# Optimization experiments

Hardware: AMD Instinct MI355X
Metric: run time of the kernel (lower is better)

## Reference

```python
import jax, jax.numpy as jnp
import numpy as np

B, T, D, H, K, V, W = 2, 2048, 1024, 16, 64, 64, 256
BANK = 64
CUE = 50250
EPS = 1e-6
SCALE = K ** -0.5
LOCAL_SCALE = 0.3
ROPE_BASE = 10000.0


def setup_inputs() -> dict:
    key = jax.random.key(0)
    ks = jax.random.split(key, 13)
    s = 0.02
    return {
        "x": jax.random.normal(ks[0], (B, T, D), jnp.float32),
        "gdn_state": jax.random.normal(ks[1], (B, H, K, V), jnp.float32),
        "input_ids": jax.random.randint(ks[2], (B, T), 0, 50320),
        "key_bank": jax.random.normal(ks[3], (H, BANK, K), jnp.float32),
        "norm_w": jnp.ones((D,), jnp.float32),
        "wq": jax.random.normal(ks[4], (D, D), jnp.float32) * s,
        "wk": jax.random.normal(ks[5], (D, D), jnp.float32) * s,
        "wv": jax.random.normal(ks[6], (D, D), jnp.float32) * s,
        "wo": jax.random.normal(ks[7], (D, D), jnp.float32) * s,
        "w_gq": jax.random.normal(ks[8], (H * K, D), jnp.float32) * s,
        "w_ro": jax.random.normal(ks[9], (D, H * V), jnp.float32) * s,
        "w_gate": jax.random.normal(ks[10], (H, D), jnp.float32) * s,
        "b_gate": jnp.ones((H,), jnp.float32),
    }


def _rope(u):
    # u: [B, T, H, K]
    inv_freq = 1.0 / (ROPE_BASE ** (jnp.arange(0, K, 2, dtype=jnp.float32) / K))
    t = jnp.arange(T, dtype=jnp.float32)
    freqs = t[:, None] * inv_freq[None, :]            # [T, K/2]
    emb = jnp.concatenate([freqs, freqs], axis=-1)    # [T, K]
    cos = jnp.cos(emb)[None, :, None, :]
    sin = jnp.sin(emb)[None, :, None, :]
    u1, u2 = u[..., : K // 2], u[..., K // 2 :]
    rotated = jnp.concatenate([-u2, u1], axis=-1)
    return u * cos + rotated * sin


def reference(x, gdn_state, input_ids, key_bank, norm_w, wq, wk, wv, wo,
              w_gq, w_ro, w_gate, b_gate):
    # RMSNorm
    rms = jnp.sqrt(jnp.mean(x * x, axis=-1, keepdims=True) + EPS)
    x_norm = x / rms * norm_w

    # QKV projections -> [B, T, H, K]
    q = (x_norm @ wq.T).reshape(B, T, H, K)
    k = (x_norm @ wk.T).reshape(B, T, H, K)
    v = (x_norm @ wv.T).reshape(B, T, H, K)
    q = _rope(q)
    k = _rope(k)

    # Causal sliding-window attention (PyTorch fallback math: full TxT + band mask)
    scores = jnp.einsum("bthk,bshk->bhts", q, k) * SCALE  # [B, H, T, T]
    i = jnp.arange(T)
    allowed = (i[None, :] <= i[:, None]) & (i[None, :] >= i[:, None] - W)  # [T, T]
    scores = jnp.where(allowed[None, None], scores, jnp.float32(-jnp.inf))
    probs = jax.nn.softmax(scores, axis=-1)
    local = jnp.einsum("bhts,bshv->bthv", probs, v).reshape(B, T, D)
    local = LOCAL_SCALE * (local @ wo.T)  # eval path: local_scale * o_proj(local_out)

    # Global retrieval from GDN state
    q_g = (x_norm @ w_gq.T).reshape(B, T, H, K)
    # CUE token override: positions with input_ids == CUE + idx use key_bank[:, idx, :]
    idx = input_ids - CUE                              # [B, T]
    valid = (idx >= 0) & (idx < BANK)
    ci = jnp.clip(idx, 0, BANK - 1)
    gathered = key_bank.transpose(1, 0, 2)[ci]         # [B, T, H, K]
    q_g = jnp.where(valid[..., None, None], gathered, q_g)

    retrieved = jnp.einsum("bhkv,bthk->bthv", gdn_state, q_g).reshape(B, T, H * V)
    retrieval_out = retrieved @ w_ro.T                 # [B, T, D]
    gate = jax.nn.sigmoid(x_norm @ w_gate.T + b_gate)  # [B, T, H]
    retrieval_out = jnp.mean(gate, axis=-1, keepdims=True) * retrieval_out

    return x + local + retrieval_out
```

## Files before the change

### kernel.cpp

```cpp
#include <hip/hip_runtime.h>
#include <cstddef>

typedef __bf16 bf16_t;
typedef __bf16 bf16x8 __attribute__((ext_vector_type(8)));
typedef __bf16 bf16x4 __attribute__((ext_vector_type(4)));
typedef float  f32x4  __attribute__((ext_vector_type(4)));

__global__ __launch_bounds__(256) void rmsnorm_gate(const float* __restrict__ x,
                                                    const float* __restrict__ w,
                                                    const float* __restrict__ wg,
                                                    const float* __restrict__ bg,
                                                    bf16_t* __restrict__ xn,
                                                    float* __restrict__ gm) {
  int t = blockIdx.x;
  int tid = threadIdx.x;
  int wave = tid >> 6, lane = tid & 63;
  const f32x4* row = (const f32x4*)(x + (size_t)t * 1024);
  f32x4 v = row[tid];
  float ss = v[0]*v[0] + v[1]*v[1] + v[2]*v[2] + v[3]*v[3];
  #pragma unroll
  for (int off = 32; off >= 1; off >>= 1) ss += __shfl_xor(ss, off);
  __shared__ float red[4];
  __shared__ float gred[4][16];
  if (lane == 0) red[wave] = ss;
  __syncthreads();
  float tot = red[0] + red[1] + red[2] + red[3];
  float rinv = rsqrtf(tot * (1.0f / 1024.0f) + 1e-6f);
  f32x4 wv = ((const f32x4*)w)[tid];
  float xnv[4];
  bf16x4 o;
  #pragma unroll
  for (int i = 0; i < 4; ++i) { xnv[i] = v[i] * rinv * wv[i]; o[i] = (bf16_t)xnv[i]; }
  *(bf16x4*)(xn + (size_t)t * 1024 + tid * 4) = o;
  float ga[16];
  #pragma unroll
  for (int h = 0; h < 16; ++h) {
    f32x4 wgh = ((const f32x4*)(wg + h * 1024))[tid];
    ga[h] = xnv[0]*wgh[0] + xnv[1]*wgh[1] + xnv[2]*wgh[2] + xnv[3]*wgh[3];
  }
  #pragma unroll
  for (int h = 0; h < 16; ++h) {
    #pragma unroll
    for (int off = 32; off >= 1; off >>= 1) ga[h] += __shfl_xor(ga[h], off);
  }
  if (lane < 16) gred[wave][lane] = ga[lane];
  __syncthreads();
  if (tid < 16) {
    float s = gred[0][tid] + gred[1][tid] + gred[2][tid] + gred[3][tid];
    float sig = 1.0f / (1.0f + __expf(-(s + bg[tid])));
    #pragma unroll
    for (int off = 8; off >= 1; off >>= 1) sig += __shfl_xor(sig, off);
    if (tid == 0) gm[t] = sig * (1.0f / 16.0f);
  }
}

struct CvtArgs { const float* s[6]; bf16_t* d[6]; int stride[6]; float scale[6]; };
__global__ __launch_bounds__(256) void convert6(CvtArgs a) {
  int m = blockIdx.y;
  const f32x4* src = (const f32x4*)a.s[m];
  int i = blockIdx.x * 256 + threadIdx.x;
  f32x4 v = src[i];
  int rrow = i >> 8;
  int col = (i & 255) * 4;
  float sc = a.scale[m];
  bf16x4 o;
  #pragma unroll
  for (int j = 0; j < 4; ++j) o[j] = (bf16_t)(v[j] * sc);
  *(bf16x4*)(a.d[m] + (size_t)rrow * a.stride[m] + col) = o;
}

struct GemmSeg { const bf16_t* a; const bf16_t* w; void* c; int mode; };
struct GemmCfg { GemmSeg seg[4]; const float* x; };
#define LDSK 40
template<int KD>
__global__ __launch_bounds__(256, 2) void gemm_bt(GemmCfg cfg) {
  __shared__ bf16_t As[128 * LDSK];
  __shared__ bf16_t Bs[128 * LDSK];
  int seg = blockIdx.x >> 3;
  const bf16_t* __restrict__ A = cfg.seg[seg].a;
  const bf16_t* __restrict__ W = cfg.seg[seg].w;
  int m0 = blockIdx.y * 128;
  int n0 = (blockIdx.x & 7) * 128;
  int tid = threadIdx.x;
  int lane = tid & 63, wave = tid >> 6;
  int wm = (wave >> 1) * 64, wn = (wave & 1) * 64;
  int l16 = lane & 15, quad = lane >> 4;
  f32x4 acc[4][4] = {};
  for (int k0 = 0; k0 < KD; k0 += 32) {
    __syncthreads();
    #pragma unroll
    for (int c = 0; c < 2; ++c) {
      int ci = tid + c * 256;
      int r = ci >> 2;
      int ko = (ci & 3) * 8;
      *(uint4*)&As[r * LDSK + ko] = *(const uint4*)&A[(size_t)(m0 + r) * KD + k0 + ko];
      *(uint4*)&Bs[r * LDSK + ko] = *(const uint4*)&W[(size_t)(n0 + r) * KD + k0 + ko];
    }
    __syncthreads();
    bf16x8 af[4], bfr[4];
    #pragma unroll
    for (int i = 0; i < 4; ++i) {
      af[i]  = *(const bf16x8*)&As[(wm + i * 16 + l16) * LDSK + quad * 8];
      bfr[i] = *(const bf16x8*)&Bs[(wn + i * 16 + l16) * LDSK + quad * 8];
    }
    #pragma unroll
    for (int i = 0; i < 4; ++i)
      #pragma unroll
      for (int j = 0; j < 4; ++j)
        acc[i][j] = __builtin_amdgcn_mfma_f32_16x16x32_bf16(af[i], bfr[j], acc[i][j], 0, 0, 0);
  }
  int mode = cfg.seg[seg].mode;
  if (mode == 1) {
    #pragma unroll
    for (int jp = 0; jp < 2; ++jp) {
      int d = jp * 16 + l16;
      float inv = exp2f((float)d * -0.41524101186092029f);
      #pragma unroll
      for (int i = 0; i < 4; ++i)
        #pragma unroll
        for (int r = 0; r < 4; ++r) {
          int tseq = (m0 + wm + i * 16 + quad * 4 + r) & 2047;
          float sn, cs;
          sincosf((float)tseq * inv, &sn, &cs);
          float v1 = acc[i][jp][r], v2 = acc[i][jp + 2][r];
          acc[i][jp][r]     = v1 * cs - v2 * sn;
          acc[i][jp + 2][r] = v2 * cs + v1 * sn;
        }
    }
  }
  if (mode == 2) {
    float* C = (float*)cfg.seg[seg].c;
    const float* X = cfg.x;
    #pragma unroll
    for (int i = 0; i < 4; ++i)
      #pragma unroll
      for (int j = 0; j < 4; ++j) {
        int row = m0 + wm + i * 16 + quad * 4;
        int col = n0 + wn + j * 16 + l16;
        #pragma unroll
        for (int r = 0; r < 4; ++r) {
          size_t idx = (size_t)(row + r) * 1024 + col;
          C[idx] = X[idx] + acc[i][j][r];
        }
      }
  } else {
    bf16_t* C = (bf16_t*)cfg.seg[seg].c;
    #pragma unroll
    for (int i = 0; i < 4; ++i)
      #pragma unroll
      for (int j = 0; j < 4; ++j) {
        int row = m0 + wm + i * 16 + quad * 4;
        int col = n0 + wn + j * 16 + l16;
        #pragma unroll
        for (int r = 0; r < 4; ++r)
          C[(size_t)(row + r) * 1024 + col] = (bf16_t)acc[i][j][r];
      }
  }
}

__global__ __launch_bounds__(256) void attn_mfma(const bf16_t* __restrict__ qb,
                                                 const bf16_t* __restrict__ kb,
                                                 const bf16_t* __restrict__ vb,
                                                 bf16_t* __restrict__ ab2) {
  __shared__ bf16_t Ks[64 * 72];
  __shared__ bf16_t Vt[64 * 72];
  __shared__ float  Os[4][16 * 68];
  int blk = blockIdx.x;
  int tcb = blk & 31;
  int h = (blk >> 5) & 15;
  int b = blk >> 9;
  int t0 = tcb * 64;
  int tid = threadIdx.x;
  int wv = tid >> 6, lane = tid & 63;
  int l15 = lane & 15, quad = lane >> 4;
  int tq0 = t0 + wv * 16;
  int t = tq0 + l15;
  int lo = t - 256; if (lo < 0) lo = 0;

  const bf16_t* qptr = qb + (((size_t)(b * 2048 + t) * 16) + h) * 64;
  bf16x8 qf0 = *(const bf16x8*)(qptr + quad * 8);
  bf16x8 qf1 = *(const bf16x8*)(qptr + 32 + quad * 8);

  f32x4 acc[4] = {};
  float mrun = -1e30f, lrun = 0.f;

  for (int c = 0; c < 5; ++c) {
    int s0 = t0 - 256 + c * 64;
    __syncthreads();
    #pragma unroll
    for (int it = 0; it < 2; ++it) {
      int task = tid + it * 256;
      int key = task >> 3, dseg = task & 7;
      int s = s0 + key; s = s < 0 ? 0 : (s > 2047 ? 2047 : s);
      *(bf16x8*)&Ks[key * 72 + dseg * 8] =
        *(const bf16x8*)(kb + (((size_t)(b * 2048 + s) * 16) + h) * 64 + dseg * 8);
    }
    {
      int vseg = tid & 7, kp = tid >> 3;
      int sA = s0 + 2 * kp, sB = sA + 1;
      sA = sA < 0 ? 0 : (sA > 2047 ? 2047 : sA);
      sB = sB < 0 ? 0 : (sB > 2047 ? 2047 : sB);
      bf16x8 va = *(const bf16x8*)(vb + (((size_t)(b * 2048 + sA) * 16) + h) * 64 + vseg * 8);
      bf16x8 vbv = *(const bf16x8*)(vb + (((size_t)(b * 2048 + sB) * 16) + h) * 64 + vseg * 8);
      #pragma unroll
      for (int j = 0; j < 8; ++j) {
        union { bf16_t h2[2]; unsigned int u; } pk;
        pk.h2[0] = va[j]; pk.h2[1] = vbv[j];
        *(unsigned int*)&Vt[(vseg * 8 + j) * 72 + 2 * kp] = pk.u;
      }
    }
    __syncthreads();
    #pragma unroll
    for (int p = 0; p < 2; ++p) {
      int sbase = s0 + p * 32;
      if (sbase > tq0 + 15 || sbase + 31 < tq0 - 256 || sbase + 31 < 0) continue;
      int kl = p * 32;
      bf16x8 ka0  = *(const bf16x8*)&Ks[(kl + l15) * 72 + quad * 8];
      bf16x8 ka0b = *(const bf16x8*)&Ks[(kl + l15) * 72 + 32 + quad * 8];
      bf16x8 ka1  = *(const bf16x8*)&Ks[(kl + 16 + l15) * 72 + quad * 8];
      bf16x8 ka1b = *(const bf16x8*)&Ks[(kl + 16 + l15) * 72 + 32 + quad * 8];
      f32x4 c0 = {}, c1 = {};
      c0 = __builtin_amdgcn_mfma_f32_16x16x32_bf16(ka0,  qf0, c0, 0, 0, 0);
      c0 = __builtin_amdgcn_mfma_f32_16x16x32_bf16(ka0b, qf1, c0, 0, 0, 0);
      c1 = __builtin_amdgcn_mfma_f32_16x16x32_bf16(ka1,  qf0, c1, 0, 0, 0);
      c1 = __builtin_amdgcn_mfma_f32_16x16x32_bf16(ka1b, qf1, c1, 0, 0, 0);
      float p0[4], p1[4];
      float mx = -1e30f;
      #pragma unroll
      for (int r = 0; r < 4; ++r) {
        int sK0 = sbase + quad * 4 + r;
        int sK1 = sK0 + 16;
        float v0 = (sK0 >= lo && sK0 <= t) ? c0[r] * 0.125f : -1e30f;
        float v1 = (sK1 >= lo && sK1 <= t) ? c1[r] * 0.125f : -1e30f;
        p0[r] = v0; p1[r] = v1;
        mx = fmaxf(mx, fmaxf(v0, v1));
      }
      mx = fmaxf(mx, __shfl_xor(mx, 16));
      mx = fmaxf(mx, __shfl_xor(mx, 32));
      float mnew = fmaxf(mrun, mx);
      float alpha = __expf(mrun - mnew);
      float rs = 0.f;
      #pragma unroll
      for (int r = 0; r < 4; ++r) {
        float e0 = (p0[r] > -1e29f) ? __expf(p0[r] - mnew) : 0.f;
        float e1 = (p1[r] > -1e29f) ? __expf(p1[r] - mnew) : 0.f;
        p0[r] = e0; p1[r] = e1;
        rs += e0 + e1;
      }
      rs += __shfl_xor(rs, 16);
      rs += __shfl_xor(rs, 32);
      mrun = mnew;
      lrun = lrun * alpha + rs;
      #pragma unroll
      for (int vt = 0; vt < 4; ++vt)
        #pragma unroll
        for (int r = 0; r < 4; ++r) acc[vt][r] *= alpha;
      union { bf16x4 v; int2 i2; } pka, pkb;
      #pragma unroll
      for (int r = 0; r < 4; ++r) { pka.v[r] = (bf16_t)p0[r]; pkb.v[r] = (bf16_t)p1[r]; }
      int sel = quad >> 1;
      int base = l15 + ((quad & 1) << 5);
      int a0 = __shfl(pka.i2.x, base),      b0 = __shfl(pkb.i2.x, base);
      int a1 = __shfl(pka.i2.y, base),      b1 = __shfl(pkb.i2.y, base);
      int a2 = __shfl(pka.i2.x, base + 16), b2 = __shfl(pkb.i2.x, base + 16);
      int a3 = __shfl(pka.i2.y, base + 16), b3 = __shfl(pkb.i2.y, base + 16);
      union { int4 i4; bf16x8 v; } pf;
      pf.i4.x = sel ? b0 : a0;
      pf.i4.y = sel ? b1 : a1;
      pf.i4.z = sel ? b2 : a2;
      pf.i4.w = sel ? b3 : a3;
      #pragma unroll
      for (int vt = 0; vt < 4; ++vt) {
        bf16x8 vfr = *(const bf16x8*)&Vt[(vt * 16 + l15) * 72 + kl + quad * 8];
        acc[vt] = __builtin_amdgcn_mfma_f32_16x16x32_bf16(vfr, pf.v, acc[vt], 0, 0, 0);
      }
    }
  }
  float rl = 1.0f / lrun;
  float* myOs = &Os[wv][0];
  #pragma unroll
  for (int vt = 0; vt < 4; ++vt)
    #pragma unroll
    for (int r = 0; r < 4; ++r)
      myOs[l15 * 68 + vt * 16 + quad * 4 + r] = acc[vt][r] * rl;
  __syncthreads();
  #pragma unroll
  for (int q = 0; q < 16; ++q) {
    float v = myOs[q * 68 + lane];
    ab2[(size_t)(b * 2048 + tq0 + q) * 2048 + h * 64 + lane] = (bf16_t)v;
  }
}

__global__ __launch_bounds__(256, 2) void retrieval_kernel(const bf16_t* __restrict__ qgb,
                                                           const int* __restrict__ ids,
                                                           const float* __restrict__ bank,
                                                           const float* __restrict__ gdn,
                                                           const float* __restrict__ gm,
                                                           bf16_t* __restrict__ ab2) {
  __shared__ float G[64 * 64];
  int blk = blockIdx.x;
  int tc = blk & 7;
  int h = (blk >> 3) & 15;
  int b = blk >> 7;
  int tid = threadIdx.x;
  const f32x4* gsrc = (const f32x4*)(gdn + (size_t)(b * 16 + h) * 4096);
  #pragma unroll
  for (int it = 0; it < 4; ++it)
    ((f32x4*)G)[tid + it * 256] = gsrc[tid + it * 256];
  __syncthreads();
  int t = tc * 256 + tid;
  int id = ids[b * 2048 + t] - 50250;
  bool valid = (id >= 0) && (id < 64);
  const bf16_t* qrow = qgb + (((size_t)(b * 2048 + t) * 16) + h) * 64;
  const float* krow = bank + (size_t)(h * 64 + (valid ? id : 0)) * 64;
  float acc[64];
  #pragma unroll
  for (int v = 0; v < 64; ++v) acc[v] = 0.f;
  for (int k = 0; k < 64; ++k) {
    float qv = valid ? krow[k] : (float)qrow[k];
    const f32x4* gr = (const f32x4*)&G[k * 64];
    #pragma unroll
    for (int i = 0; i < 16; ++i) {
      f32x4 gv = gr[i];
      acc[i * 4 + 0] += qv * gv[0];
      acc[i * 4 + 1] += qv * gv[1];
      acc[i * 4 + 2] += qv * gv[2];
      acc[i * 4 + 3] += qv * gv[3];
    }
  }
  float g = gm[b * 2048 + t];
  bf16_t* orow = ab2 + (size_t)(b * 2048 + t) * 2048 + 1024 + h * 64;
  #pragma unroll
  for (int i = 0; i < 8; ++i) {
    bf16x8 ov;
    #pragma unroll
    for (int j = 0; j < 8; ++j) ov[j] = (bf16_t)(acc[i * 8 + j] * g);
    *(bf16x8*)(orow + i * 8) = ov;
  }
}

extern "C" void kernel_launch(void* const* d_in, const int* in_sizes, int n_in,
                              void* d_out, int out_size, void* d_ws, size_t ws_size,
                              hipStream_t stream) {
  const float* x        = (const float*)d_in[0];
  const float* gdn      = (const float*)d_in[1];
  const int*   ids      = (const int*)d_in[2];
  const float* key_bank = (const float*)d_in[3];
  const float* norm_w   = (const float*)d_in[4];
  const float* wq       = (const float*)d_in[5];
  const float* wk       = (const float*)d_in[6];
  const float* wv       = (const float*)d_in[7];
  const float* wo       = (const float*)d_in[8];
  const float* w_gq     = (const float*)d_in[9];
  const float* w_ro     = (const float*)d_in[10];
  const float* w_gate   = (const float*)d_in[11];
  const float* b_gate   = (const float*)d_in[12];

  char* p = (char*)d_ws;
  auto alloc = [&](size_t bytes) { char* r = p; p += (bytes + 255) & ~(size_t)255; return r; };
  const size_t ACT = (size_t)4096 * 1024 * 2;
  const size_t WTB = (size_t)1024 * 1024 * 2;
  bf16_t* xn_b   = (bf16_t*)alloc(ACT);
  bf16_t* wq_b   = (bf16_t*)alloc(WTB);
  bf16_t* wk_b   = (bf16_t*)alloc(WTB);
  bf16_t* wv_b   = (bf16_t*)alloc(WTB);
  bf16_t* wgq_b  = (bf16_t*)alloc(WTB);
  bf16_t* wcat   = (bf16_t*)alloc(WTB * 2);
  bf16_t* qb     = (bf16_t*)alloc(ACT);
  bf16_t* kb     = (bf16_t*)alloc(ACT);
  bf16_t* vb     = (bf16_t*)alloc(ACT);
  bf16_t* qgb    = (bf16_t*)alloc(ACT);
  bf16_t* ab2    = (bf16_t*)alloc(ACT * 2);
  float*  gmean  = (float*)alloc(4096 * 4);

  CvtArgs ca;
  ca.s[0] = wq;   ca.d[0] = wq_b;        ca.stride[0] = 1024; ca.scale[0] = 1.0f;
  ca.s[1] = wk;   ca.d[1] = wk_b;        ca.stride[1] = 1024; ca.scale[1] = 1.0f;
  ca.s[2] = wv;   ca.d[2] = wv_b;        ca.stride[2] = 1024; ca.scale[2] = 1.0f;
  ca.s[3] = w_gq; ca.d[3] = wgq_b;       ca.stride[3] = 1024; ca.scale[3] = 1.0f;
  ca.s[4] = wo;   ca.d[4] = wcat;        ca.stride[4] = 2048; ca.scale[4] = 0.3f;
  ca.s[5] = w_ro; ca.d[5] = wcat + 1024; ca.stride[5] = 2048; ca.scale[5] = 1.0f;
  convert6<<<dim3(1024, 6), 256, 0, stream>>>(ca);
  rmsnorm_gate<<<4096, 256, 0, stream>>>(x, norm_w, w_gate, b_gate, xn_b, gmean);

  GemmCfg g4;
  g4.seg[0] = {xn_b, wq_b,  (void*)qb,  1};
  g4.seg[1] = {xn_b, wk_b,  (void*)kb,  1};
  g4.seg[2] = {xn_b, wv_b,  (void*)vb,  0};
  g4.seg[3] = {xn_b, wgq_b, (void*)qgb, 0};
  g4.x = nullptr;
  gemm_bt<1024><<<dim3(32, 32), 256, 0, stream>>>(g4);

  attn_mfma<<<1024, 256, 0, stream>>>(qb, kb, vb, ab2);
  retrieval_kernel<<<256, 256, 0, stream>>>(qgb, ids, key_bank, gdn, gmean, ab2);

  GemmCfg gf;
  gf.seg[0] = {ab2, wcat, d_out, 2};
  gf.seg[1] = gf.seg[0];
  gf.seg[2] = gf.seg[0];
  gf.seg[3] = gf.seg[0];
  gf.x = x;
  gemm_bt<2048><<<dim3(8, 32), 256, 0, stream>>>(gf);
}
```

Baseline: 285.4 us.

## Precompute RoPE table, template GEMM mode, split QKV launch, shrink output tile

```diff
diff --git a/kernel.cpp b/kernel.cpp
--- a/kernel.cpp
+++ b/kernel.cpp
@@ -69,70 +69,85 @@
   *(bf16x4*)(a.d[m] + (size_t)rrow * a.stride[m] + col) = o;
 }
 
-struct GemmSeg { const bf16_t* a; const bf16_t* w; void* c; int mode; };
-struct GemmCfg { GemmSeg seg[4]; const float* x; };
+__global__ __launch_bounds__(256) void rope_table(float2* __restrict__ tab) {
+  int i = blockIdx.x * 256 + threadIdx.x;
+  int t = i >> 5, d = i & 31;
+  float inv = exp2f((float)d * -0.41524101186092029f);
+  float sn, cs;
+  sincosf((float)t * inv, &sn, &cs);
+  tab[i] = make_float2(cs, sn);
+}
+
+struct GemmSeg { const bf16_t* a; const bf16_t* w; void* c; };
+struct GemmCfg { GemmSeg seg[2]; const float* x; const float2* rope; };
 #define LDSK 40
-template<int KD>
+template<int KD, int MODE, int TM>
 __global__ __launch_bounds__(256, 2) void gemm_bt(GemmCfg cfg) {
-  __shared__ bf16_t As[128 * LDSK];
+  constexpr int RM = TM / 32;
+  __shared__ bf16_t As[TM * LDSK];
   __shared__ bf16_t Bs[128 * LDSK];
   int seg = blockIdx.x >> 3;
   const bf16_t* __restrict__ A = cfg.seg[seg].a;
   const bf16_t* __restrict__ W = cfg.seg[seg].w;
-  int m0 = blockIdx.y * 128;
+  int m0 = blockIdx.y * TM;
   int n0 = (blockIdx.x & 7) * 128;
   int tid = threadIdx.x;
   int lane = tid & 63, wave = tid >> 6;
-  int wm = (wave >> 1) * 64, wn = (wave & 1) * 64;
+  int wm = (wave >> 1) * (RM * 16), wn = (wave & 1) * 64;
   int l16 = lane & 15, quad = lane >> 4;
-  f32x4 acc[4][4] = {};
+  f32x4 acc[RM][4] = {};
   for (int k0 = 0; k0 < KD; k0 += 32) {
     __syncthreads();
+    #pragma unroll
+    for (int c = 0; c < TM / 64; ++c) {
+      int ci = tid + c * 256;
+      int r = ci >> 2;
+      int ko = (ci & 3) * 8;
+      *(uint4*)&As[r * LDSK + ko] = *(const uint4*)&A[(size_t)(m0 + r) * KD + k0 + ko];
+    }
     #pragma unroll
     for (int c = 0; c < 2; ++c) {
       int ci = tid + c * 256;
       int r = ci >> 2;
       int ko = (ci & 3) * 8;
-      *(uint4*)&As[r * LDSK + ko] = *(const uint4*)&A[(size_t)(m0 + r) * KD + k0 + ko];
       *(uint4*)&Bs[r * LDSK + ko] = *(const uint4*)&W[(size_t)(n0 + r) * KD + k0 + ko];
     }
     __syncthreads();
-    bf16x8 af[4], bfr[4];
-    #pragma unroll
-    for (int i = 0; i < 4; ++i) {
+    bf16x8 af[RM], bfr[4];
+    #pragma unroll
+    for (int i = 0; i < RM; ++i)
       af[i]  = *(const bf16x8*)&As[(wm + i * 16 + l16) * LDSK + quad * 8];
-      bfr[i] = *(const bf16x8*)&Bs[(wn + i * 16 + l16) * LDSK + quad * 8];
-    }
-    #pragma unroll
-    for (int i = 0; i < 4; ++i)
+    #pragma unroll
+    for (int j = 0; j < 4; ++j)
+      bfr[j] = *(const bf16x8*)&Bs[(wn + j * 16 + l16) * LDSK + quad * 8];
+    #pragma unroll
+    for (int i = 0; i < RM; ++i)
       #pragma unroll
       for (int j = 0; j < 4; ++j)
         acc[i][j] = __builtin_amdgcn_mfma_f32_16x16x32_bf16(af[i], bfr[j], acc[i][j], 0, 0, 0);
   }
-  int mode = cfg.seg[seg].mode;
-  if (mode == 1) {
+  if (MODE == 1) {
+    const float2* tab = cfg.rope;
     #pragma unroll
     for (int jp = 0; jp < 2; ++jp) {
       int d = jp * 16 + l16;
-      float inv = exp2f((float)d * -0.41524101186092029f);
-      #pragma unroll
-      for (int i = 0; i < 4; ++i)
+      #pragma unroll
+      for (int i = 0; i < RM; ++i)
         #pragma unroll
         for (int r = 0; r < 4; ++r) {
           int tseq = (m0 + wm + i * 16 + quad * 4 + r) & 2047;
-          float sn, cs;
-          sincosf((float)tseq * inv, &sn, &cs);
+          float2 cz = tab[(tseq << 5) + d];
           float v1 = acc[i][jp][r], v2 = acc[i][jp + 2][r];
-          acc[i][jp][r]     = v1 * cs - v2 * sn;
-          acc[i][jp + 2][r] = v2 * cs + v1 * sn;
+          acc[i][jp][r]     = v1 * cz.x - v2 * cz.y;
+          acc[i][jp + 2][r] = v2 * cz.x + v1 * cz.y;
         }
     }
   }
-  if (mode == 2) {
+  if (MODE == 2) {
     float* C = (float*)cfg.seg[seg].c;
     const float* X = cfg.x;
     #pragma unroll
-    for (int i = 0; i < 4; ++i)
+    for (int i = 0; i < RM; ++i)
       #pragma unroll
       for (int j = 0; j < 4; ++j) {
         int row = m0 + wm + i * 16 + quad * 4;
@@ -146,7 +161,7 @@
   } else {
     bf16_t* C = (bf16_t*)cfg.seg[seg].c;
     #pragma unroll
-    for (int i = 0; i < 4; ++i)
+    for (int i = 0; i < RM; ++i)
       #pragma unroll
       for (int j = 0; j < 4; ++j) {
         int row = m0 + wm + i * 16 + quad * 4;
@@ -372,6 +387,7 @@
   bf16_t* qgb    = (bf16_t*)alloc(ACT);
   bf16_t* ab2    = (bf16_t*)alloc(ACT * 2);
   float*  gmean  = (float*)alloc(4096 * 4);
+  float2* rtab   = (float2*)alloc(2048 * 32 * sizeof(float2));
 
   CvtArgs ca;
   ca.s[0] = wq;   ca.d[0] = wq_b;        ca.stride[0] = 1024; ca.scale[0] = 1.0f;
@@ -381,24 +397,27 @@
   ca.s[4] = wo;   ca.d[4] = wcat;        ca.stride[4] = 2048; ca.scale[4] = 0.3f;
   ca.s[5] = w_ro; ca.d[5] = wcat + 1024; ca.stride[5] = 2048; ca.scale[5] = 1.0f;
   convert6<<<dim3(1024, 6), 256, 0, stream>>>(ca);
+  rope_table<<<256, 256, 0, stream>>>(rtab);
   rmsnorm_gate<<<4096, 256, 0, stream>>>(x, norm_w, w_gate, b_gate, xn_b, gmean);
 
-  GemmCfg g4;
-  g4.seg[0] = {xn_b, wq_b,  (void*)qb,  1};
-  g4.seg[1] = {xn_b, wk_b,  (void*)kb,  1};
-  g4.seg[2] = {xn_b, wv_b,  (void*)vb,  0};
-  g4.seg[3] = {xn_b, wgq_b, (void*)qgb, 0};
-  g4.x = nullptr;
-  gemm_bt<1024><<<dim3(32, 32), 256, 0, stream>>>(g4);
+  GemmCfg gqk;
+  gqk.seg[0] = {xn_b, wq_b, (void*)qb};
+  gqk.seg[1] = {xn_b, wk_b, (void*)kb};
+  gqk.x = nullptr; gqk.rope = rtab;
+  gemm_bt<1024, 1, 128><<<dim3(16, 32), 256, 0, stream>>>(gqk);
+
+  GemmCfg gvq;
+  gvq.seg[0] = {xn_b, wv_b,  (void*)vb};
+  gvq.seg[1] = {xn_b, wgq_b, (void*)qgb};
+  gvq.x = nullptr; gvq.rope = nullptr;
+  gemm_bt<1024, 0, 128><<<dim3(16, 32), 256, 0, stream>>>(gvq);
 
   attn_mfma<<<1024, 256, 0, stream>>>(qb, kb, vb, ab2);
   retrieval_kernel<<<256, 256, 0, stream>>>(qgb, ids, key_bank, gdn, gmean, ab2);
 
   GemmCfg gf;
-  gf.seg[0] = {ab2, wcat, d_out, 2};
+  gf.seg[0] = {ab2, wcat, d_out};
   gf.seg[1] = gf.seg[0];
-  gf.seg[2] = gf.seg[0];
-  gf.seg[3] = gf.seg[0];
-  gf.x = x;
-  gemm_bt<2048><<<dim3(8, 32), 256, 0, stream>>>(gf);
-}
+  gf.x = x; gf.rope = nullptr;
+  gemm_bt<2048, 2, 64><<<dim3(8, 64), 256, 0, stream>>>(gf);
+}
```

Result: no change. 281.8 us (-1.3%).

## Fuse prep kernels, merge attention with retrieval, split output GEMM with atomics

Applied to the files above, without the earlier changes.

```diff
diff --git a/kernel.cpp b/kernel.cpp
--- a/kernel.cpp
+++ b/kernel.cpp
@@ -6,27 +6,52 @@
 typedef __bf16 bf16x4 __attribute__((ext_vector_type(4)));
 typedef float  f32x4  __attribute__((ext_vector_type(4)));
 
-__global__ __launch_bounds__(256) void rmsnorm_gate(const float* __restrict__ x,
-                                                    const float* __restrict__ w,
-                                                    const float* __restrict__ wg,
-                                                    const float* __restrict__ bg,
-                                                    bf16_t* __restrict__ xn,
-                                                    float* __restrict__ gm) {
-  int t = blockIdx.x;
+struct CvtArgs { const float* s[6]; bf16_t* d[6]; float scale[6]; };
+__global__ __launch_bounds__(256) void prep_kernel(CvtArgs ca,
+                                                   const float* __restrict__ x,
+                                                   const float* __restrict__ nw,
+                                                   const float* __restrict__ wg,
+                                                   const float* __restrict__ bg,
+                                                   bf16_t* __restrict__ xn,
+                                                   float* __restrict__ gm,
+                                                   float2* __restrict__ rtab,
+                                                   float* __restrict__ dout) {
+  __shared__ float red[4];
+  __shared__ float gred[4][16];
+  int bid = blockIdx.x;
   int tid = threadIdx.x;
+  if (bid < 6144) {
+    int m = bid >> 10;
+    int i = (bid & 1023) * 256 + tid;
+    f32x4 v = ((const f32x4*)ca.s[m])[i];
+    float sc = ca.scale[m];
+    bf16x4 o;
+    #pragma unroll
+    for (int j = 0; j < 4; ++j) o[j] = (bf16_t)(v[j] * sc);
+    *(bf16x4*)(ca.d[m] + (size_t)i * 4) = o;
+    return;
+  }
+  if (bid < 6400) {
+    int i = (bid - 6144) * 256 + tid;
+    int t = i >> 5, d = i & 31;
+    float inv = exp2f((float)d * -0.41524101186092029f);
+    float sn, cs;
+    sincosf((float)t * inv, &sn, &cs);
+    rtab[i] = make_float2(cs, sn);
+    return;
+  }
+  int t = bid - 6400;
   int wave = tid >> 6, lane = tid & 63;
-  const f32x4* row = (const f32x4*)(x + (size_t)t * 1024);
-  f32x4 v = row[tid];
+  f32x4 v = ((const f32x4*)(x + (size_t)t * 1024))[tid];
+  ((f32x4*)(dout + (size_t)t * 1024))[tid] = v;
   float ss = v[0]*v[0] + v[1]*v[1] + v[2]*v[2] + v[3]*v[3];
   #pragma unroll
   for (int off = 32; off >= 1; off >>= 1) ss += __shfl_xor(ss, off);
-  __shared__ float red[4];
-  __shared__ float gred[4][16];
   if (lane == 0) red[wave] = ss;
   __syncthreads();
   float tot = red[0] + red[1] + red[2] + red[3];
   float rinv = rsqrtf(tot * (1.0f / 1024.0f) + 1e-6f);
-  f32x4 wv = ((const f32x4*)w)[tid];
+  f32x4 wv = ((const f32x4*)nw)[tid];
   float xnv[4];
   bf16x4 o;
   #pragma unroll
@@ -54,23 +79,8 @@
   }
 }
 
-struct CvtArgs { const float* s[6]; bf16_t* d[6]; int stride[6]; float scale[6]; };
-__global__ __launch_bounds__(256) void convert6(CvtArgs a) {
-  int m = blockIdx.y;
-  const f32x4* src = (const f32x4*)a.s[m];
-  int i = blockIdx.x * 256 + threadIdx.x;
-  f32x4 v = src[i];
-  int rrow = i >> 8;
-  int col = (i & 255) * 4;
-  float sc = a.scale[m];
-  bf16x4 o;
-  #pragma unroll
-  for (int j = 0; j < 4; ++j) o[j] = (bf16_t)(v[j] * sc);
-  *(bf16x4*)(a.d[m] + (size_t)rrow * a.stride[m] + col) = o;
-}
-
 struct GemmSeg { const bf16_t* a; const bf16_t* w; void* c; int mode; };
-struct GemmCfg { GemmSeg seg[4]; const float* x; };
+struct GemmCfg { GemmSeg seg[4]; const float2* rope; };
 #define LDSK 40
 template<int KD>
 __global__ __launch_bounds__(256, 2) void gemm_bt(GemmCfg cfg) {
@@ -111,26 +121,24 @@
   }
   int mode = cfg.seg[seg].mode;
   if (mode == 1) {
+    const float2* tab = cfg.rope;
     #pragma unroll
     for (int jp = 0; jp < 2; ++jp) {
       int d = jp * 16 + l16;
-      float inv = exp2f((float)d * -0.41524101186092029f);
       #pragma unroll
       for (int i = 0; i < 4; ++i)
         #pragma unroll
         for (int r = 0; r < 4; ++r) {
           int tseq = (m0 + wm + i * 16 + quad * 4 + r) & 2047;
-          float sn, cs;
-          sincosf((float)tseq * inv, &sn, &cs);
+          float2 cz = tab[(tseq << 5) + d];
           float v1 = acc[i][jp][r], v2 = acc[i][jp + 2][r];
-          acc[i][jp][r]     = v1 * cs - v2 * sn;
-          acc[i][jp + 2][r] = v2 * cs + v1 * sn;
+          acc[i][jp][r]     = v1 * cz.x - v2 * cz.y;
+          acc[i][jp + 2][r] = v2 * cz.x + v1 * cz.y;
         }
     }
   }
-  if (mode == 2) {
+  if (mode == 3) {
     float* C = (float*)cfg.seg[seg].c;
-    const float* X = cfg.x;
     #pragma unroll
     for (int i = 0; i < 4; ++i)
       #pragma unroll
@@ -138,10 +146,8 @@
         int row = m0 + wm + i * 16 + quad * 4;
         int col = n0 + wn + j * 16 + l16;
         #pragma unroll
-        for (int r = 0; r < 4; ++r) {
-          size_t idx = (size_t)(row + r) * 1024 + col;
-          C[idx] = X[idx] + acc[i][j][r];
-        }
+        for (int r = 0; r < 4; ++r)
+          unsafeAtomicAdd(&C[(size_t)(row + r) * 1024 + col], acc[i][j][r]);
       }
   } else {
     bf16_t* C = (bf16_t*)cfg.seg[seg].c;
@@ -158,184 +164,185 @@
   }
 }
 
-__global__ __launch_bounds__(256) void attn_mfma(const bf16_t* __restrict__ qb,
+__global__ __launch_bounds__(256) void attn_retr(const bf16_t* __restrict__ qb,
                                                  const bf16_t* __restrict__ kb,
                                                  const bf16_t* __restrict__ vb,
-                                                 bf16_t* __restrict__ ab2) {
-  __shared__ bf16_t Ks[64 * 72];
-  __shared__ bf16_t Vt[64 * 72];
-  __shared__ float  Os[4][16 * 68];
-  int blk = blockIdx.x;
-  int tcb = blk & 31;
-  int h = (blk >> 5) & 15;
-  int b = blk >> 9;
-  int t0 = tcb * 64;
+                                                 const bf16_t* __restrict__ qgb,
+                                                 const int* __restrict__ ids,
+                                                 const float* __restrict__ bank,
+                                                 const float* __restrict__ gdn,
+                                                 const float* __restrict__ gm,
+                                                 bf16_t* __restrict__ attn_b,
+                                                 bf16_t* __restrict__ retr_b) {
+  __shared__ alignas(16) char smem[35840];
   int tid = threadIdx.x;
-  int wv = tid >> 6, lane = tid & 63;
-  int l15 = lane & 15, quad = lane >> 4;
-  int tq0 = t0 + wv * 16;
-  int t = tq0 + l15;
-  int lo = t - 256; if (lo < 0) lo = 0;
-
-  const bf16_t* qptr = qb + (((size_t)(b * 2048 + t) * 16) + h) * 64;
-  bf16x8 qf0 = *(const bf16x8*)(qptr + quad * 8);
-  bf16x8 qf1 = *(const bf16x8*)(qptr + 32 + quad * 8);
-
-  f32x4 acc[4] = {};
-  float mrun = -1e30f, lrun = 0.f;
-
-  for (int c = 0; c < 5; ++c) {
-    int s0 = t0 - 256 + c * 64;
+  if (blockIdx.x < 1024) {
+    bf16_t* Ks = (bf16_t*)smem;
+    bf16_t* Vt = (bf16_t*)(smem + 9216);
+    float*  Oa = (float*)(smem + 18432);
+    int blk = blockIdx.x;
+    int tcb = blk & 31;
+    int h = (blk >> 5) & 15;
+    int b = blk >> 9;
+    int t0 = tcb * 64;
+    int wv = tid >> 6, lane = tid & 63;
+    int l15 = lane & 15, quad = lane >> 4;
+    int tq0 = t0 + wv * 16;
+    int t = tq0 + l15;
+    int lo = t - 256; if (lo < 0) lo = 0;
+
+    const bf16_t* qptr = qb + (((size_t)(b * 2048 + t) * 16) + h) * 64;
+    bf16x8 qf0 = *(const bf16x8*)(qptr + quad * 8);
+    bf16x8 qf1 = *(const bf16x8*)(qptr + 32 + quad * 8);
+
+    f32x4 acc[4] = {};
+    float mrun = -1e30f, lrun = 0.f;
+
+    for (int c = 0; c < 5; ++c) {
+      int s0 = t0 - 256 + c * 64;
+      __syncthreads();
+      #pragma unroll
+      for (int it = 0; it < 2; ++it) {
+        int task = tid + it * 256;
+        int key = task >> 3, dseg = task & 7;
+        int s = s0 + key; s = s < 0 ? 0 : (s > 2047 ? 2047 : s);
+        *(bf16x8*)&Ks[key * 72 + dseg * 8] =
+          *(const bf16x8*)(kb + (((size_t)(b * 2048 + s) * 16) + h) * 64 + dseg * 8);
+      }
+      {
+        int vseg = tid & 7, kp = tid >> 3;
+        int sA = s0 + 2 * kp, sB = sA + 1;
+        sA = sA < 0 ? 0 : (sA > 2047 ? 2047 : sA);
+        sB = sB < 0 ? 0 : (sB > 2047 ? 2047 : sB);
+        bf16x8 va = *(const bf16x8*)(vb + (((size_t)(b * 2048 + sA) * 16) + h) * 64 + vseg * 8);
+        bf16x8 vbv = *(const bf16x8*)(vb + (((size_t)(b * 2048 + sB) * 16) + h) * 64 + vseg * 8);
+        #pragma unroll
+        for (int j = 0; j < 8; ++j) {
+          union { bf16_t h2[2]; unsigned int u; } pk;
+          pk.h2[0] = va[j]; pk.h2[1] = vbv[j];
+          *(unsigned int*)&Vt[(vseg * 8 + j) * 72 + 2 * kp] = pk.u;
+        }
+      }
+      __syncthreads();
+      #pragma unroll
+      for (int p = 0; p < 2; ++p) {
+        int sbase = s0 + p * 32;
+        if (sbase > tq0 + 15 || sbase + 31 < tq0 - 256 || sbase + 31 < 0) continue;
+        int kl = p * 32;
+        bf16x8 ka0  = *(const bf16x8*)&Ks[(kl + l15) * 72 + quad * 8];
+        bf16x8 ka0b = *(const bf16x8*)&Ks[(kl + l15) * 72 + 32 + quad * 8];
+        bf16x8 ka1  = *(const bf16x8*)&Ks[(kl + 16 + l15) * 72 + quad * 8];
+        bf16x8 ka1b = *(const bf16x8*)&Ks[(kl + 16 + l15) * 72 + 32 + quad * 8];
+        f32x4 c0 = {}, c1 = {};
+        c0 = __builtin_amdgcn_mfma_f32_16x16x32_bf16(ka0,  qf0, c0, 0, 0, 0);
+        c0 = __builtin_amdgcn_mfma_f32_16x16x32_bf16(ka0b, qf1, c0, 0, 0, 0);
+        c1 = __builtin_amdgcn_mfma_f32_16x16x32_bf16(ka1,  qf0, c1, 0, 0, 0);
+        c1 = __builtin_amdgcn_mfma_f32_16x16x32_bf16(ka1b, qf1, c1, 0, 0, 0);
+        float p0[4], p1[4];
+        float mx = -1e30f;
+        #pragma unroll
+        for (int r = 0; r < 4; ++r) {
+          int sK0 = sbase + quad * 4 + r;
+          int sK1 = sK0 + 16;
+          float v0 = (sK0 >= lo && sK0 <= t) ? c0[r] * 0.125f : -1e30f;
+          float v1 = (sK1 >= lo && sK1 <= t) ? c1[r] * 0.125f : -1e30f;
+          p0[r] = v0; p1[r] = v1;
+          mx = fmaxf(mx, fmaxf(v0, v1));
+        }
+        mx = fmaxf(mx, __shfl_xor(mx, 16));
+        mx = fmaxf(mx, __shfl_xor(mx, 32));
+        float mnew = fmaxf(mrun, mx);
+        float alpha = __expf(mrun - mnew);
+        float rs = 0.f;
+        #pragma unroll
+        for (int r = 0; r < 4; ++r) {
+          float e0 = (p0[r] > -1e29f) ? __expf(p0[r] - mnew) : 0.f;
+          float e1 = (p1[r] > -1e29f) ? __expf(p1[r] - mnew) : 0.f;
+          p0[r] = e0; p1[r] = e1;
+          rs += e0 + e1;
+        }
+        rs += __shfl_xor(rs, 16);
+        rs += __shfl_xor(rs, 32);
+        mrun = mnew;
+        lrun = lrun * alpha + rs;
+        #pragma unroll
+        for (int vt = 0; vt < 4; ++vt)
+          #pragma unroll
+          for (int r = 0; r < 4; ++r) acc[vt][r] *= alpha;
+        union { bf16x4 v; int2 i2; } pka, pkb;
+        #pragma unroll
+        for (int r = 0; r < 4; ++r) { pka.v[r] = (bf16_t)p0[r]; pkb.v[r] = (bf16_t)p1[r]; }
+        int sel = quad >> 1;
+        int base = l15 + ((quad & 1) << 5);
+        int a0 = __shfl(pka.i2.x, base),      b0 = __shfl(pkb.i2.x, base);
+        int a1 = __shfl(pka.i2.y, base),      b1 = __shfl(pkb.i2.y, base);
+        int a2 = __shfl(pka.i2.x, base + 16), b2 = __shfl(pkb.i2.x, base + 16);
+        int a3 = __shfl(pka.i2.y, base + 16), b3 = __shfl(pkb.i2.y, base + 16);
+        union { int4 i4; bf16x8 v; } pf;
+        pf.i4.x = sel ? b0 : a0;
+        pf.i4.y = sel ? b1 : a1;
+        pf.i4.z = sel ? b2 : a2;
+        pf.i4.w = sel ? b3 : a3;
+        #pragma unroll
+        for (int vt = 0; vt < 4; ++vt) {
+          bf16x8 vfr = *(const bf16x8*)&Vt[(vt * 16 + l15) * 72 + kl + quad * 8];
+          acc[vt] = __builtin_amdgcn_mfma_f32_16x16x32_bf16(vfr, pf.v, acc[vt], 0, 0, 0);
+        }
+      }
+    }
+    float rl = 1.0f / lrun;
+    float* myOs = Oa + wv * (16 * 68);
+    #pragma unroll
+    for (int vt = 0; vt < 4; ++vt)
+      #pragma unroll
+      for (int r = 0; r < 4; ++r)
+        myOs[l15 * 68 + vt * 16 + quad * 4 + r] = acc[vt][r] * rl;
     __syncthreads();
     #pragma unroll
-    for (int it = 0; it < 2; ++it) {
-      int task = tid + it * 256;
-      int key = task >> 3, dseg = task & 7;
-      int s = s0 + key; s = s < 0 ? 0 : (s > 2047 ? 2047 : s);
-      *(bf16x8*)&Ks[key * 72 + dseg * 8] =
-        *(const bf16x8*)(kb + (((size_t)(b * 2048 + s) * 16) + h) * 64 + dseg * 8);
-    }
-    {
-      int vseg = tid & 7, kp = tid >> 3;
-      int sA = s0 + 2 * kp, sB = sA + 1;
-      sA = sA < 0 ? 0 : (sA > 2047 ? 2047 : sA);
-      sB = sB < 0 ? 0 : (sB > 2047 ? 2047 : sB);
-      bf16x8 va = *(const bf16x8*)(vb + (((size_t)(b * 2048 + sA) * 16) + h) * 64 + vseg * 8);
-      bf16x8 vbv = *(const bf16x8*)(vb + (((size_t)(b * 2048 + sB) * 16) + h) * 64 + vseg * 8);
-      #pragma unroll
-      for (int j = 0; j < 8; ++j) {
-        union { bf16_t h2[2]; unsigned int u; } pk;
-        pk.h2[0] = va[j]; pk.h2[1] = vbv[j];
-        *(unsigned int*)&Vt[(vseg * 8 + j) * 72 + 2 * kp] = pk.u;
-      }
-    }
+    for (int q = 0; q < 16; ++q) {
+      float v = myOs[q * 68 + lane];
+      attn_b[(size_t)(b * 2048 + tq0 + q) * 1024 + h * 64 + lane] = (bf16_t)v;
+    }
+  } else {
+    float* G = (float*)smem;
+    int blk = blockIdx.x - 1024;
+    int tc = blk & 7;
+    int h = (blk >> 3) & 15;
+    int b = blk >> 7;
+    const f32x4* gsrc = (const f32x4*)(gdn + (size_t)(b * 16 + h) * 4096);
+    #pragma unroll
+    for (int it = 0; it < 4; ++it)
+      ((f32x4*)G)[tid + it * 256] = gsrc[tid + it * 256];
     __syncthreads();
-    #pragma unroll
-    for (int p = 0; p < 2; ++p) {
-      int sbase = s0 + p * 32;
-      if (sbase > tq0 + 15 || sbase + 31 < tq0 - 256 || sbase + 31 < 0) continue;
-      int kl = p * 32;
-      bf16x8 ka0  = *(const bf16x8*)&Ks[(kl + l15) * 72 + quad * 8];
-      bf16x8 ka0b = *(const bf16x8*)&Ks[(kl + l15) * 72 + 32 + quad * 8];
-      bf16x8 ka1  = *(const bf16x8*)&Ks[(kl + 16 + l15) * 72 + quad * 8];
-      bf16x8 ka1b = *(const bf16x8*)&Ks[(kl + 16 + l15) * 72 + 32 + quad * 8];
-      f32x4 c0 = {}, c1 = {};
-      c0 = __builtin_amdgcn_mfma_f32_16x16x32_bf16(ka0,  qf0, c0, 0, 0, 0);
-      c0 = __builtin_amdgcn_mfma_f32_16x16x32_bf16(ka0b, qf1, c0, 0, 0, 0);
-      c1 = __builtin_amdgcn_mfma_f32_16x16x32_bf16(ka1,  qf0, c1, 0, 0, 0);
-      c1 = __builtin_amdgcn_mfma_f32_16x16x32_bf16(ka1b, qf1, c1, 0, 0, 0);
-      float p0[4], p1[4];
-      float mx = -1e30f;
-      #pragma unroll
-      for (int r = 0; r < 4; ++r) {
-        int sK0 = sbase + quad * 4 + r;
-        int sK1 = sK0 + 16;
-        float v0 = (sK0 >= lo && sK0 <= t) ? c0[r] * 0.125f : -1e30f;
-        float v1 = (sK1 >= lo && sK1 <= t) ? c1[r] * 0.125f : -1e30f;
-        p0[r] = v0; p1[r] = v1;
-        mx = fmaxf(mx, fmaxf(v0, v1));
-      }
-      mx = fmaxf(mx, __shfl_xor(mx, 16));
-      mx = fmaxf(mx, __shfl_xor(mx, 32));
-      float mnew = fmaxf(mrun, mx);
-      float alpha = __expf(mrun - mnew);
-      float rs = 0.f;
-      #pragma unroll
-      for (int r = 0; r < 4; ++r) {
-        float e0 = (p0[r] > -1e29f) ? __expf(p0[r] - mnew) : 0.f;
-        float e1 = (p1[r] > -1e29f) ? __expf(p1[r] - mnew) : 0.f;
-        p0[r] = e0; p1[r] = e1;
-        rs += e0 + e1;
-      }
-      rs += __shfl_xor(rs, 16);
-      rs += __shfl_xor(rs, 32);
-      mrun = mnew;
-      lrun = lrun * alpha + rs;
-      #pragma unroll
-      for (int vt = 0; vt < 4; ++vt)
-        #pragma unroll
-        for (int r = 0; r < 4; ++r) acc[vt][r] *= alpha;
-      union { bf16x4 v; int2 i2; } pka, pkb;
-      #pragma unroll
-      for (int r = 0; r < 4; ++r) { pka.v[r] = (bf16_t)p0[r]; pkb.v[r] = (bf16_t)p1[r]; }
-      int sel = quad >> 1;
-      int base = l15 + ((quad & 1) << 5);
-      int a0 = __shfl(pka.i2.x, base),      b0 = __shfl(pkb.i2.x, base);
-      int a1 = __shfl(pka.i2.y, base),      b1 = __shfl(pkb.i2.y, base);
-      int a2 = __shfl(pka.i2.x, base + 16), b2 = __shfl(pkb.i2.x, base + 16);
-      int a3 = __shfl(pka.i2.y, base + 16), b3 = __shfl(pkb.i2.y, base + 16);
-      union { int4 i4; bf16x8 v; } pf;
-      pf.i4.x = sel ? b0 : a0;
-      pf.i4.y = sel ? b1 : a1;
-      pf.i4.z = sel ? b2 : a2;
-      pf.i4.w = sel ? b3 : a3;
-      #pragma unroll
-      for (int vt = 0; vt < 4; ++vt) {
-        bf16x8 vfr = *(const bf16x8*)&Vt[(vt * 16 + l15) * 72 + kl + quad * 8];
-        acc[vt] = __builtin_amdgcn_mfma_f32_16x16x32_bf16(vfr, pf.v, acc[vt], 0, 0, 0);
-      }
-    }
-  }
-  float rl = 1.0f / lrun;
-  float* myOs = &Os[wv][0];
-  #pragma unroll
-  for (int vt = 0; vt < 4; ++vt)
-    #pragma unroll
-    for (int r = 0; r < 4; ++r)
-      myOs[l15 * 68 + vt * 16 + quad * 4 + r] = acc[vt][r] * rl;
-  __syncthreads();
-  #pragma unroll
-  for (int q = 0; q < 16; ++q) {
-    float v = myOs[q * 68 + lane];
-    ab2[(size_t)(b * 2048 + tq0 + q) * 2048 + h * 64 + lane] = (bf16_t)v;
-  }
-}
-
-__global__ __launch_bounds__(256, 2) void retrieval_kernel(const bf16_t* __restrict__ qgb,
-                                                           const int* __restrict__ ids,
-                                                           const float* __restrict__ bank,
-                                                           const float* __restrict__ gdn,
-                                                           const float* __restrict__ gm,
-                                                           bf16_t* __restrict__ ab2) {
-  __shared__ float G[64 * 64];
-  int blk = blockIdx.x;
-  int tc = blk & 7;
-  int h = (blk >> 3) & 15;
-  int b = blk >> 7;
-  int tid = threadIdx.x;
-  const f32x4* gsrc = (const f32x4*)(gdn + (size_t)(b * 16 + h) * 4096);
-  #pragma unroll
-  for (int it = 0; it < 4; ++it)
-    ((f32x4*)G)[tid + it * 256] = gsrc[tid + it * 256];
-  __syncthreads();
-  int t = tc * 256 + tid;
-  int id = ids[b * 2048 + t] - 50250;
-  bool valid = (id >= 0) && (id < 64);
-  const bf16_t* qrow = qgb + (((size_t)(b * 2048 + t) * 16) + h) * 64;
-  const float* krow = bank + (size_t)(h * 64 + (valid ? id : 0)) * 64;
-  float acc[64];
-  #pragma unroll
-  for (int v = 0; v < 64; ++v) acc[v] = 0.f;
-  for (int k = 0; k < 64; ++k) {
-    float qv = valid ? krow[k] : (float)qrow[k];
-    const f32x4* gr = (const f32x4*)&G[k * 64];
-    #pragma unroll
-    for (int i = 0; i < 16; ++i) {
-      f32x4 gv = gr[i];
-      acc[i * 4 + 0] += qv * gv[0];
-      acc[i * 4 + 1] += qv * gv[1];
-      acc[i * 4 + 2] += qv * gv[2];
-      acc[i * 4 + 3] += qv * gv[3];
-    }
-  }
-  float g = gm[b * 2048 + t];
-  bf16_t* orow = ab2 + (size_t)(b * 2048 + t) * 2048 + 1024 + h * 64;
-  #pragma unroll
-  for (int i = 0; i < 8; ++i) {
-    bf16x8 ov;
-    #pragma unroll
-    for (int j = 0; j < 8; ++j) ov[j] = (bf16_t)(acc[i * 8 + j] * g);
-    *(bf16x8*)(orow + i * 8) = ov;
+    int t = tc * 256 + tid;
+    int id = ids[b * 2048 + t] - 50250;
+    bool valid = (id >= 0) && (id < 64);
+    const bf16_t* qrow = qgb + (((size_t)(b * 2048 + t) * 16) + h) * 64;
+    const float* krow = bank + (size_t)(h * 64 + (valid ? id : 0)) * 64;
+    float acc[64];
+    #pragma unroll
+    for (int v = 0; v < 64; ++v) acc[v] = 0.f;
+    for (int k = 0; k < 64; ++k) {
+      float qv = valid ? krow[k] : (float)qrow[k];
+      const f32x4* gr = (const f32x4*)&G[k * 64];
+      #pragma unroll
+      for (int i = 0; i < 16; ++i) {
+        f32x4 gv = gr[i];
+        acc[i * 4 + 0] += qv * gv[0];
+        acc[i * 4 + 1] += qv * gv[1];
+        acc[i * 4 + 2] += qv * gv[2];
+        acc[i * 4 + 3] += qv * gv[3];
+      }
+    }
+    float g = gm[b * 2048 + t];
+    bf16_t* orow = retr_b + (size_t)(b * 2048 + t) * 1024 + h * 64;
+    #pragma unroll
+    for (int i = 0; i < 8; ++i) {
+      bf16x8 ov;
+      #pragma unroll
+      for (int j = 0; j < 8; ++j) ov[j] = (bf16_t)(acc[i * 8 + j] * g);
+      *(bf16x8*)(orow + i * 8) = ov;
+    }
   }
 }
 
@@ -365,40 +372,43 @@
   bf16_t* wk_b   = (bf16_t*)alloc(WTB);
   bf16_t* wv_b   = (bf16_t*)alloc(WTB);
   bf16_t* wgq_b  = (bf16_t*)alloc(WTB);
-  bf16_t* wcat   = (bf16_t*)alloc(WTB * 2);
+  bf16_t* wo_b   = (bf16_t*)alloc(WTB);
+  bf16_t* wro_b  = (bf16_t*)alloc(WTB);
   bf16_t* qb     = (bf16_t*)alloc(ACT);
   bf16_t* kb     = (bf16_t*)alloc(ACT);
   bf16_t* vb     = (bf16_t*)alloc(ACT);
   bf16_t* qgb    = (bf16_t*)alloc(ACT);
-  bf16_t* ab2    = (bf16_t*)alloc(ACT * 2);
+  bf16_t* attn_b = (bf16_t*)alloc(ACT);
+  bf16_t* retr_b = (bf16_t*)alloc(ACT);
   float*  gmean  = (float*)alloc(4096 * 4);
+  float2* rtab   = (float2*)alloc(2048 * 32 * sizeof(float2));
 
   CvtArgs ca;
-  ca.s[0] = wq;   ca.d[0] = wq_b;        ca.stride[0] = 1024; ca.scale[0] = 1.0f;
-  ca.s[1] = wk;   ca.d[1] = wk_b;        ca.stride[1] = 1024; ca.scale[1] = 1.0f;
-  ca.s[2] = wv;   ca.d[2] = wv_b;        ca.stride[2] = 1024; ca.scale[2] = 1.0f;
-  ca.s[3] = w_gq; ca.d[3] = wgq_b;       ca.stride[3] = 1024; ca.scale[3] = 1.0f;
-  ca.s[4] = wo;   ca.d[4] = wcat;        ca.stride[4] = 2048; ca.scale[4] = 0.3f;
-  ca.s[5] = w_ro; ca.d[5] = wcat + 1024; ca.stride[5] = 2048; ca.scale[5] = 1.0f;
-  convert6<<<dim3(1024, 6), 256, 0, stream>>>(ca);
-  rmsnorm_gate<<<4096, 256, 0, stream>>>(x, norm_w, w_gate, b_gate, xn_b, gmean);
+  ca.s[0] = wq;   ca.d[0] = wq_b;   ca.scale[0] = 1.0f;
+  ca.s[1] = wk;   ca.d[1] = wk_b;   ca.scale[1] = 1.0f;
+  ca.s[2] = wv;   ca.d[2] = wv_b;   ca.scale[2] = 1.0f;
+  ca.s[3] = w_gq; ca.d[3] = wgq_b;  ca.scale[3] = 1.0f;
+  ca.s[4] = wo;   ca.d[4] = wo_b;   ca.scale[4] = 0.3f;
+  ca.s[5] = w_ro; ca.d[5] = wro_b;  ca.scale[5] = 1.0f;
+  prep_kernel<<<10496, 256, 0, stream>>>(ca, x, norm_w, w_gate, b_gate,
+                                         xn_b, gmean, rtab, (float*)d_out);
 
   GemmCfg g4;
   g4.seg[0] = {xn_b, wq_b,  (void*)qb,  1};
   g4.seg[1] = {xn_b, wk_b,  (void*)kb,  1};
   g4.seg[2] = {xn_b, wv_b,  (void*)vb,  0};
   g4.seg[3] = {xn_b, wgq_b, (void*)qgb, 0};
-  g4.x = nullptr;
+  g4.rope = rtab;
   gemm_bt<1024><<<dim3(32, 32), 256, 0, stream>>>(g4);
 
-  attn_mfma<<<1024, 256, 0, stream>>>(qb, kb, vb, ab2);
-  retrieval_kernel<<<256, 256, 0, stream>>>(qgb, ids, key_bank, gdn, gmean, ab2);
+  attn_retr<<<1280, 256, 0, stream>>>(qb, kb, vb, qgb, ids, key_bank, gdn,
+                                      gmean, attn_b, retr_b);
 
   GemmCfg gf;
-  gf.seg[0] = {ab2, wcat, d_out, 2};
-  gf.seg[1] = gf.seg[0];
+  gf.seg[0] = {attn_b, wo_b,  d_out, 3};
+  gf.seg[1] = {retr_b, wro_b, d_out, 3};
   gf.seg[2] = gf.seg[0];
   gf.seg[3] = gf.seg[0];
-  gf.x = x;
-  gemm_bt<2048><<<dim3(8, 32), 256, 0, stream>>>(gf);
+  gf.rope = nullptr;
+  gemm_bt<1024><<<dim3(16, 32), 256, 0, stream>>>(gf);
 }
```

Result: faster. 263.1 us (-7.8%).
